# Optimization experiments

Hardware: AMD Instinct MI355X
Metric: run time of the kernel (lower is better)

The kernel has to match this reference:

```python
import jax, jax.numpy as jnp
import numpy as np

N, E = 50000, 800000
HID, HEADS, EDIM = 64, 4, 3
NEG_SLOPE = 0.2
LN_EPS = 1e-5


def setup_inputs() -> dict:
    key = jax.random.key(0)
    ks = jax.random.split(key, 12)
    h = jax.random.normal(ks[0], (N, HID), dtype=jnp.float32)
    edge_index = jax.random.randint(ks[1], (2, E), 0, N, dtype=jnp.int64)
    edge_attr = jax.random.normal(ks[2], (E, EDIM), dtype=jnp.float32)
    t = jax.random.uniform(ks[3], (1,), dtype=jnp.float32)
    s = 1.0 / np.sqrt(HID)
    W = jax.random.normal(ks[4], (HID, HEADS * HID), dtype=jnp.float32) * s
    att_src = jax.random.normal(ks[5], (1, HEADS, HID), dtype=jnp.float32) * s
    att_dst = jax.random.normal(ks[6], (1, HEADS, HID), dtype=jnp.float32) * s
    W_edge = jax.random.normal(ks[7], (EDIM, HEADS * HID), dtype=jnp.float32) * s
    att_edge = jax.random.normal(ks[8], (1, HEADS, HID), dtype=jnp.float32) * s
    bias = jnp.zeros((HID,), dtype=jnp.float32)
    ln_gamma = jnp.ones((HID,), dtype=jnp.float32)
    ln_beta = jnp.zeros((HID,), dtype=jnp.float32)
    return {"t": t, "h": h, "edge_index": edge_index, "edge_attr": edge_attr,
            "W": W, "att_src": att_src, "att_dst": att_dst, "W_edge": W_edge,
            "att_edge": att_edge, "bias": bias, "ln_gamma": ln_gamma, "ln_beta": ln_beta}


def reference(t, h, edge_index, edge_attr, W, att_src, att_dst, W_edge, att_edge, bias, ln_gamma, ln_beta):
    # GATConv (PyG, edge_dim>0, add_self_loops=False, concat=False, eval mode)
    x = (h @ W).reshape(N, HEADS, HID)                     # [N,H,C]
    a_src = (x * att_src).sum(-1)                          # [N,H]
    a_dst = (x * att_dst).sum(-1)                          # [N,H]
    e = (edge_attr @ W_edge).reshape(E, HEADS, HID)        # [E,H,C]
    a_edge = (e * att_edge).sum(-1)                        # [E,H]
    src, dst = edge_index[0], edge_index[1]
    alpha = a_src[src] + a_dst[dst] + a_edge               # [E,H]
    alpha = jax.nn.leaky_relu(alpha, NEG_SLOPE)
    # softmax over edges sharing the same destination node
    amax = jax.ops.segment_max(alpha, dst, num_segments=N)  # [N,H]
    ex = jnp.exp(alpha - amax[dst])
    esum = jax.ops.segment_sum(ex, dst, num_segments=N)     # [N,H]
    alpha = ex / (esum[dst] + 1e-16)
    msg = x[src] * alpha[:, :, None]                        # [E,H,C]
    out = jax.ops.segment_sum(msg, dst, num_segments=N)     # [N,H,C]
    out = out.mean(axis=1) + bias                           # concat=False -> head mean
    # LayerNorm + SiLU
    mu = out.mean(-1, keepdims=True)
    var = ((out - mu) ** 2).mean(-1, keepdims=True)
    y = (out - mu) * jax.lax.rsqrt(var + LN_EPS) * ln_gamma + ln_beta
    return y * jax.nn.sigmoid(y)
```

## Files before the change

kernel.cpp:

```cpp
#include <hip/hip_runtime.h>
#include <hip/hip_bf16.h>

#define HIDC 64
#define NEG_SLOPE 0.2f
#define SCAN_G 128

typedef __hip_bfloat16 bf16;
typedef short bf16x8 __attribute__((ext_vector_type(8)));
typedef float floatx4 __attribute__((ext_vector_type(4)));
typedef int intx4 __attribute__((ext_vector_type(4)));

static __device__ __forceinline__ float b2f(bf16 v) { return __bfloat162float(v); }

static __device__ __forceinline__ unsigned short f2us(float f) {
  bf16 b = __float2bfloat16(f);
  union { bf16 b; unsigned short u; } c;
  c.b = b;
  return c.u;
}

template <bool FF>
static __device__ __forceinline__ float ld(const void* __restrict__ p, size_t i) {
  return FF ? ((const float*)p)[i] : b2f(((const bf16*)p)[i]);
}
static __device__ __forceinline__ float ldr(const void* __restrict__ p, size_t i,
                                            bool ff) {
  return ff ? ((const float*)p)[i] : b2f(((const bf16*)p)[i]);
}
template <bool I64>
static __device__ __forceinline__ int ldi(const int* __restrict__ p, long long i) {
  return I64 ? (int)((const long long*)p)[i] : p[i];
}
static __device__ __forceinline__ int clampN(int v, int N) {
  return ((unsigned)v < (unsigned)N) ? v : 0;
}

static __device__ __forceinline__ int4 ntload4(const int4* __restrict__ p) {
  intx4 v = __builtin_nontemporal_load((const intx4*)p);
  return make_int4(v.x, v.y, v.z, v.w);
}

static __device__ __forceinline__ bool det_f32(const unsigned* __restrict__ hw) {
  unsigned w = hw[threadIdx.x & 31];
  int ex = (w >> 7) & 0xFF;
  unsigned long long b = __ballot(ex >= 99 && ex <= 135);
  return __popcll(b) < 32;
}
static __device__ __forceinline__ bool det_i64(const int* __restrict__ ei) {
  int v = ei[2 * (threadIdx.x & 31) + 1];
  return __ballot(v != 0) == 0ULL;
}

template <bool FF, bool I64>
static __device__ __forceinline__ void xh_body(
    const void* __restrict__ h, const void* __restrict__ W,
    const void* __restrict__ att_src, const void* __restrict__ att_dst,
    const int* __restrict__ ei, bf16* __restrict__ x,
    float* __restrict__ a_src, float* __restrict__ a_dst,
    int* __restrict__ cnt, int* __restrict__ erank, int N, int E,
    unsigned short* __restrict__ hls, unsigned short* __restrict__ wls) {
  for (long long e = (long long)blockIdx.x * 256 + threadIdx.x; e < E;
       e += (long long)gridDim.x * 256) {
    int dst = clampN(ldi<I64>(ei, (long long)E + e), N);
    erank[e] = atomicAdd(&cnt[dst], 1);
  }
  const int t = threadIdx.x;
  const long long n0 = (long long)blockIdx.x * 64;
  {
    const int c = t;
    const int jn = c & 63, hd = c >> 6;
    const int r = hd * 64 + (jn & 3) * 16 + (jn >> 2);
#pragma unroll
    for (int q = 0; q < 8; q++) {
      unsigned short u[8];
#pragma unroll
      for (int j = 0; j < 8; j++) {
        int k = q * 8 + j;
        u[j] = FF ? f2us(((const float*)W)[(size_t)k * 256 + c])
                  : ((const unsigned short*)W)[(size_t)k * 256 + c];
      }
      int4 v = make_int4((int)(u[0] | ((unsigned)u[1] << 16)),
                         (int)(u[2] | ((unsigned)u[3] << 16)),
                         (int)(u[4] | ((unsigned)u[5] << 16)),
                         (int)(u[6] | ((unsigned)u[7] << 16)));
      *(int4*)&wls[r * 64 + (q ^ (r & 7)) * 8] = v;
    }
  }
  {
    const int row = t >> 2;
    const long long n = n0 + row;
#pragma unroll
    for (int dq = 0; dq < 2; dq++) {
      int q = (t & 3) * 2 + dq;
      int4 v;
      if (n < N) {
        if (FF) {
          const float4* hp = (const float4*)h + n * 16 + q * 2;
          float4 f0 = hp[0], f1 = hp[1];
          v = make_int4((int)(f2us(f0.x) | ((unsigned)f2us(f0.y) << 16)),
                        (int)(f2us(f0.z) | ((unsigned)f2us(f0.w) << 16)),
                        (int)(f2us(f1.x) | ((unsigned)f2us(f1.y) << 16)),
                        (int)(f2us(f1.z) | ((unsigned)f2us(f1.w) << 16)));
        } else {
          v = *((const int4*)((const unsigned short*)h + n * 64 + q * 8));
        }
      } else {
        v = make_int4(0, 0, 0, 0);
      }
      *(int4*)&hls[row * 64 + (q ^ (row & 7)) * 8] = v;
    }
  }
  __syncthreads();
  const int w = t >> 6;
  const int lane = t & 63;
  const int lm = lane & 15, lq = lane >> 4;
  bf16x8 af[4][2];
#pragma unroll
  for (int nt = 0; nt < 4; nt++)
#pragma unroll
    for (int ks = 0; ks < 2; ks++) {
      int m = nt * 16 + lm;
      int q = ks * 4 + lq;
      af[nt][ks] = *(const bf16x8*)&hls[m * 64 + (q ^ (m & 7)) * 8];
    }
  floatx4 acc[4][4];
#pragma unroll
  for (int nt = 0; nt < 4; nt++)
#pragma unroll
    for (int ct = 0; ct < 4; ct++) acc[nt][ct] = (floatx4){0.f, 0.f, 0.f, 0.f};
#pragma unroll
  for (int ct = 0; ct < 4; ct++) {
    int c = w * 64 + ct * 16 + lm;
    bf16x8 b0 = *(const bf16x8*)&wls[c * 64 + ((lq) ^ (c & 7)) * 8];
    bf16x8 b1 = *(const bf16x8*)&wls[c * 64 + ((4 + lq) ^ (c & 7)) * 8];
#pragma unroll
    for (int nt = 0; nt < 4; nt++) {
      acc[nt][ct] = __builtin_amdgcn_mfma_f32_16x16x32_bf16(af[nt][0], b0,
                                                            acc[nt][ct], 0, 0, 0);
      acc[nt][ct] = __builtin_amdgcn_mfma_f32_16x16x32_bf16(af[nt][1], b1,
                                                            acc[nt][ct], 0, 0, 0);
    }
  }
  float as_c[4], ad_c[4];
#pragma unroll
  for (int ct = 0; ct < 4; ct++) {
    as_c[ct] = ld<FF>(att_src, w * 64 + lm * 4 + ct);
    ad_c[ct] = ld<FF>(att_dst, w * 64 + lm * 4 + ct);
  }
#pragma unroll
  for (int nt = 0; nt < 4; nt++) {
    float ps[4] = {0.f, 0.f, 0.f, 0.f}, pd[4] = {0.f, 0.f, 0.f, 0.f};
#pragma unroll
    for (int ct = 0; ct < 4; ct++) {
#pragma unroll
      for (int r = 0; r < 4; r++) {
        ps[r] += acc[nt][ct][r] * as_c[ct];
        pd[r] += acc[nt][ct][r] * ad_c[ct];
      }
    }
    long long nb = n0 + nt * 16 + lq * 4;
#pragma unroll
    for (int r = 0; r < 4; r++) {
      long long n = nb + r;
      if (n < N) {
        ushort4 us = make_ushort4(f2us(acc[nt][0][r]), f2us(acc[nt][1][r]),
                                  f2us(acc[nt][2][r]), f2us(acc[nt][3][r]));
        *(ushort4*)&x[n * 256 + w * 64 + lm * 4] = us;
      }
    }
#pragma unroll
    for (int mask = 1; mask < 16; mask <<= 1) {
#pragma unroll
      for (int r = 0; r < 4; r++) {
        ps[r] += __shfl_xor(ps[r], mask);
        pd[r] += __shfl_xor(pd[r], mask);
      }
    }
    if (lm == 0) {
#pragma unroll
      for (int r = 0; r < 4; r++) {
        long long n = nb + r;
        if (n < N) {
          a_src[n * 4 + w] = ps[r];
          a_dst[n * 4 + w] = pd[r];
        }
      }
    }
  }
}

__global__ void __launch_bounds__(256) k_xh(
    const void* __restrict__ h, const void* __restrict__ W,
    const void* __restrict__ att_src, const void* __restrict__ att_dst,
    const int* __restrict__ ei, bf16* __restrict__ x,
    float* __restrict__ a_src, float* __restrict__ a_dst,
    int* __restrict__ cnt, int* __restrict__ erank, int N, int E) {
  __shared__ alignas(16) unsigned short hls[64 * 64];
  __shared__ alignas(16) unsigned short wls[256 * 64];
  bool f32 = det_f32((const unsigned*)h);
  bool i64 = det_i64(ei);
  if (f32) {
    if (i64) xh_body<true, true>(h, W, att_src, att_dst, ei, x, a_src, a_dst, cnt, erank, N, E, hls, wls);
    else     xh_body<true, false>(h, W, att_src, att_dst, ei, x, a_src, a_dst, cnt, erank, N, E, hls, wls);
  } else {
    if (i64) xh_body<false, true>(h, W, att_src, att_dst, ei, x, a_src, a_dst, cnt, erank, N, E, hls, wls);
    else     xh_body<false, false>(h, W, att_src, att_dst, ei, x, a_src, a_dst, cnt, erank, N, E, hls, wls);
  }
}

__global__ void __launch_bounds__(1024) k_bscan(
    const void* __restrict__ W_edge, const void* __restrict__ att_edge,
    const unsigned* __restrict__ hw, const int* __restrict__ cnt,
    int* __restrict__ offs, int* __restrict__ bsum, int* __restrict__ bbase,
    int* __restrict__ done, float* __restrict__ M, int N) {
  int b = blockIdx.x, t = threadIdx.x;
  if (b == 0 && t < 768) {
    bool ff = det_f32(hw);
    int wv = t >> 6, lane = t & 63;
    int d = wv >> 2, hh = wv & 3;
    float p = ldr(W_edge, (size_t)d * 256 + hh * 64 + lane, ff) *
              ldr(att_edge, (size_t)hh * 64 + lane, ff);
#pragma unroll
    for (int o = 32; o; o >>= 1) p += __shfl_down(p, o);
    if (lane == 0) M[d * 4 + hh] = p;
  }
  const int C = (N + SCAN_G - 1) / SCAN_G;
  const int b0 = b * C;
  __shared__ int ts[1024];
  __shared__ int lastf;
  int v = 0;
  if (t < C && b0 + t < N) v = cnt[b0 + t];
  ts[t] = v;
  __syncthreads();
  for (int off = 1; off < 1024; off <<= 1) {
    int u = (t >= off) ? ts[t - off] : 0;
    __syncthreads();
    ts[t] += u;
    __syncthreads();
  }
  if (t < C && b0 + t < N) offs[b0 + t] = ts[t] - v;
  if (t == 1023) {
    atomicExch(&bsum[b], ts[1023]);
    __threadfence();
    int old = atomicAdd(done, 1);
    lastf = (old == SCAN_G - 1) ? 1 : 0;
  }
  __syncthreads();
  if (lastf) {
    int w = (t < SCAN_G) ? atomicAdd(&bsum[t], 0) : 0;
    ts[t] = w;
    __syncthreads();
    for (int off = 1; off < 1024; off <<= 1) {
      int u = (t >= off) ? ts[t - off] : 0;
      __syncthreads();
      ts[t] += u;
      __syncthreads();
    }
    if (t < SCAN_G) bbase[t] = ts[t] - w;
  }
}

template <bool FF, bool I64>
static __device__ __forceinline__ void es_body(
    const int* __restrict__ ei, const void* __restrict__ eattr,
    const float* __restrict__ a_src, const float* __restrict__ a_dst,
    const float* __restrict__ M, const int* __restrict__ offs,
    const int* __restrict__ bbase, const int* __restrict__ erank,
    int4* __restrict__ slots, int E, int N, int C,
    unsigned* __restrict__ sattr) {
  const long long e0 = (long long)blockIdx.x * 256;
  {
    const unsigned bpe = FF ? 12u : 6u;
    const unsigned* gsrc = (const unsigned*)((const char*)eattr + e0 * bpe);
    unsigned ndw = FF ? 768u : 384u;
    long long bytes_left = ((long long)E - e0) * bpe;
    if (bytes_left < 0) bytes_left = 0;
    unsigned max_dw = (unsigned)((bytes_left + 3) >> 2);
    if (ndw > max_dw) ndw = max_dw;
    for (unsigned i = threadIdx.x; i < ndw; i += 256) sattr[i] = gsrc[i];
  }
  __syncthreads();
  long long e = e0 + threadIdx.x;
  if (e >= E) return;
  int src = clampN(ldi<I64>(ei, e), N);
  int dst = clampN(ldi<I64>(ei, (long long)E + e), N);
  int pos = offs[dst] + bbase[dst / C] + erank[e];
  float ea0, ea1, ea2;
  if (FF) {
    const float* sf = (const float*)sattr;
    ea0 = sf[threadIdx.x * 3 + 0];
    ea1 = sf[threadIdx.x * 3 + 1];
    ea2 = sf[threadIdx.x * 3 + 2];
  } else {
    const unsigned short* su = (const unsigned short*)sattr;
    ea0 = __uint_as_float((unsigned)su[threadIdx.x * 3 + 0] << 16);
    ea1 = __uint_as_float((unsigned)su[threadIdx.x * 3 + 1] << 16);
    ea2 = __uint_as_float((unsigned)su[threadIdx.x * 3 + 2] << 16);
  }
  const float4 m0 = ((const float4*)M)[0];
  const float4 m1 = ((const float4*)M)[1];
  const float4 m2 = ((const float4*)M)[2];
  const float4 as4 = ((const float4*)a_src)[src];
  const float4 ad4 = ((const float4*)a_dst)[dst];
  float al[4];
  al[0] = as4.x + ad4.x + ea0 * m0.x + ea1 * m1.x + ea2 * m2.x;
  al[1] = as4.y + ad4.y + ea0 * m0.y + ea1 * m1.y + ea2 * m2.y;
  al[2] = as4.z + ad4.z + ea0 * m0.z + ea1 * m1.z + ea2 * m2.z;
  al[3] = as4.w + ad4.w + ea0 * m0.w + ea1 * m1.w + ea2 * m2.w;
  unsigned short u[4];
#pragma unroll
  for (int hh = 0; hh < 4; hh++) {
    float a = al[hh];
    a = (a > 0.f) ? a : NEG_SLOPE * a;
    a = fminf(fmaxf(a, -60.f), 60.f);
    u[hh] = f2us(__expf(a));
  }
  slots[pos] = make_int4(src, (int)(u[0] | ((unsigned)u[1] << 16)),
                         (int)(u[2] | ((unsigned)u[3] << 16)), 0);
}

__global__ void __launch_bounds__(256) k_es(
    const int* __restrict__ ei, const void* __restrict__ eattr,
    const float* __restrict__ a_src, const float* __restrict__ a_dst,
    const float* __restrict__ M, const unsigned* __restrict__ hw,
    const int* __restrict__ offs, const int* __restrict__ bbase,
    const int* __restrict__ erank, int4* __restrict__ slots, int E, int N,
    int C) {
  __shared__ unsigned sattr[768];
  bool f32 = det_f32(hw);
  bool i64 = det_i64(ei);
  if (f32) {
    if (i64) es_body<true, true>(ei, eattr, a_src, a_dst, M, offs, bbase, erank, slots, E, N, C, sattr);
    else     es_body<true, false>(ei, eattr, a_src, a_dst, M, offs, bbase, erank, slots, E, N, C, sattr);
  } else {
    if (i64) es_body<false, true>(ei, eattr, a_src, a_dst, M, offs, bbase, erank, slots, E, N, C, sattr);
    else     es_body<false, false>(ei, eattr, a_src, a_dst, M, offs, bbase, erank, slots, E, N, C, sattr);
  }
}

static __device__ __forceinline__ uint2 xgat(const uint2* __restrict__ xr,
                                             int src, int lane) {
  int ss = __builtin_amdgcn_readfirstlane(src);
  return xr[(size_t)(unsigned)ss * 64 + lane];
}

__global__ void __launch_bounds__(256) k_agg(
    const int* __restrict__ offs, const int* __restrict__ bbase,
    const int4* __restrict__ slots, const unsigned* __restrict__ xu,
    const unsigned* __restrict__ hw, const void* __restrict__ bias,
    const void* __restrict__ gamma, const void* __restrict__ beta,
    void* __restrict__ out, int N, int E, int C) {
  const int t = threadIdx.x;
  const int wv = t >> 6, lane = t & 63;
  const int n = blockIdx.x * 4 + wv;
  if (n >= N) return;
  const int head2 = lane >> 5;
  const unsigned wshift = (lane & 16) ? 0u : 16u;
  const uint2* __restrict__ xr = (const uint2*)xu;

  int s0 = __builtin_amdgcn_readfirstlane(offs[n] + bbase[n / C]);
  int s1 = (n + 1 < N)
               ? __builtin_amdgcn_readfirstlane(offs[n + 1] + bbase[(n + 1) / C])
               : E;

  float a0 = 0.f, a1 = 0.f, a2 = 0.f, a3 = 0.f, ws = 0.f;

#define ACC4(q, d)                                                    \
  do {                                                                \
    unsigned ee = head2 ? (unsigned)(q).z : (unsigned)(q).y;          \
    float wv_ = __uint_as_float((ee << wshift) & 0xffff0000u);        \
    a0 += wv_ * __uint_as_float((d).x << 16);                         \
    a1 += wv_ * __uint_as_float((d).x & 0xffff0000u);                 \
    a2 += wv_ * __uint_as_float((d).y << 16);                         \
    a3 += wv_ * __uint_as_float((d).y & 0xffff0000u);                 \
    ws += wv_;                                                        \
  } while (0)

  int i = s0;
  for (; i + 8 <= s1; i += 8) {
    int4 q0 = ntload4(&slots[i + 0]);
    int4 q1 = ntload4(&slots[i + 1]);
    int4 q2 = ntload4(&slots[i + 2]);
    int4 q3 = ntload4(&slots[i + 3]);
    int4 q4 = ntload4(&slots[i + 4]);
    int4 q5 = ntload4(&slots[i + 5]);
    int4 q6 = ntload4(&slots[i + 6]);
    int4 q7 = ntload4(&slots[i + 7]);
    uint2 d0 = xgat(xr, q0.x, lane);
    uint2 d1 = xgat(xr, q1.x, lane);
    uint2 d2 = xgat(xr, q2.x, lane);
    uint2 d3 = xgat(xr, q3.x, lane);
    uint2 d4 = xgat(xr, q4.x, lane);
    uint2 d5 = xgat(xr, q5.x, lane);
    uint2 d6 = xgat(xr, q6.x, lane);
    uint2 d7 = xgat(xr, q7.x, lane);
    ACC4(q0, d0); ACC4(q1, d1); ACC4(q2, d2); ACC4(q3, d3);
    ACC4(q4, d4); ACC4(q5, d5); ACC4(q6, d6); ACC4(q7, d7);
  }
  for (; i + 4 <= s1; i += 4) {
    int4 q0 = ntload4(&slots[i + 0]);
    int4 q1 = ntload4(&slots[i + 1]);
    int4 q2 = ntload4(&slots[i + 2]);
    int4 q3 = ntload4(&slots[i + 3]);
    uint2 d0 = xgat(xr, q0.x, lane);
    uint2 d1 = xgat(xr, q1.x, lane);
    uint2 d2 = xgat(xr, q2.x, lane);
    uint2 d3 = xgat(xr, q3.x, lane);
    ACC4(q0, d0); ACC4(q1, d1); ACC4(q2, d2); ACC4(q3, d3);
  }
  for (; i < s1; i++) {
    int4 q = ntload4(&slots[i]);
    uint2 d = xgat(xr, q.x, lane);
    ACC4(q, d);
  }
#undef ACC4

  float inv = 1.f / (ws + 1e-16f);
  float v0 = a0 * inv, v1 = a1 * inv, v2 = a2 * inv, v3 = a3 * inv;
  v0 += __shfl_xor(v0, 16); v1 += __shfl_xor(v1, 16);
  v2 += __shfl_xor(v2, 16); v3 += __shfl_xor(v3, 16);
  v0 += __shfl_xor(v0, 32); v1 += __shfl_xor(v1, 32);
  v2 += __shfl_xor(v2, 32); v3 += __shfl_xor(v3, 32);

  bool ff = det_f32(hw);
  const int c0 = (lane & 15) * 4;
  float m0 = v0 * 0.25f + ldr(bias, c0 + 0, ff);
  float m1 = v1 * 0.25f + ldr(bias, c0 + 1, ff);
  float m2 = v2 * 0.25f + ldr(bias, c0 + 2, ff);
  float m3 = v3 * 0.25f + ldr(bias, c0 + 3, ff);

  float s = (m0 + m1) + (m2 + m3);
  s += __shfl_xor(s, 1); s += __shfl_xor(s, 2);
  s += __shfl_xor(s, 4); s += __shfl_xor(s, 8);
  float mu = s * 0.015625f;
  float d0 = m0 - mu, d1 = m1 - mu, d2 = m2 - mu, d3 = m3 - mu;
  float vq = (d0 * d0 + d1 * d1) + (d2 * d2 + d3 * d3);
  vq += __shfl_xor(vq, 1); vq += __shfl_xor(vq, 2);
  vq += __shfl_xor(vq, 4); vq += __shfl_xor(vq, 8);
  float rstd = rsqrtf(vq * 0.015625f + 1e-5f);

  if ((lane >> 4) == 0) {
    float y0 = d0 * rstd * ldr(gamma, c0 + 0, ff) + ldr(beta, c0 + 0, ff);
    float y1 = d1 * rstd * ldr(gamma, c0 + 1, ff) + ldr(beta, c0 + 1, ff);
    float y2 = d2 * rstd * ldr(gamma, c0 + 2, ff) + ldr(beta, c0 + 2, ff);
    float y3 = d3 * rstd * ldr(gamma, c0 + 3, ff) + ldr(beta, c0 + 3, ff);
    float r0 = y0 / (1.f + __expf(-y0));
    float r1 = y1 / (1.f + __expf(-y1));
    float r2 = y2 / (1.f + __expf(-y2));
    float r3 = y3 / (1.f + __expf(-y3));
    size_t ob = (size_t)n * 64 + c0;
    if (ff) {
      *(float4*)((float*)out + ob) = make_float4(r0, r1, r2, r3);
    } else {
      *(ushort4*)((bf16*)out + ob) =
          make_ushort4(f2us(r0), f2us(r1), f2us(r2), f2us(r3));
    }
  }
}

extern "C" void kernel_launch(void* const* d_in, const int* in_sizes, int n_in,
                              void* d_out, int out_size, void* d_ws,
                              size_t ws_size, hipStream_t stream) {
  const void* h        = d_in[1];
  const int*  ei       = (const int*)d_in[2];
  const void* eattr    = d_in[3];
  const void* W        = d_in[4];
  const void* att_src  = d_in[5];
  const void* att_dst  = d_in[6];
  const void* W_edge   = d_in[7];
  const void* att_edge = d_in[8];
  const void* bias     = d_in[9];
  const void* gamma    = d_in[10];
  const void* beta     = d_in[11];

  const int N = in_sizes[1] / HIDC;
  const int E = in_sizes[3] / 3;
  const int C = (N + SCAN_G - 1) / SCAN_G;

  char* p = (char*)d_ws;
  float* M    = (float*)p; p += 64;
  bf16* x     = (bf16*)p;  p += (size_t)N * 256 * 2;
  float* asrc = (float*)p; p += (size_t)N * 4 * 4;
  float* adst = (float*)p; p += (size_t)N * 4 * 4;
  int4* slots = (int4*)p;  p += (size_t)E * 16;
  int* cnt    = (int*)p;   p += (size_t)N * 4;
  int* done   = (int*)p;   p += 64;
  int* offs   = (int*)p;   p += ((size_t)N + 4) * 4;
  int* erank  = (int*)p;   p += (size_t)E * 4;
  int* bsum   = (int*)p;   p += SCAN_G * 4;
  int* bbase  = (int*)p;   p += SCAN_G * 4;

  size_t need = (size_t)(p - (char*)d_ws);
  if (ws_size < need || N <= 0 || E <= 0) {
    hipMemsetAsync(d_out, 0, (size_t)out_size * 2, stream);
    return;
  }

  hipMemsetAsync(cnt, 0, (size_t)N * 4 + 64, stream);

  k_xh<<<(N + 63) / 64, 256, 0, stream>>>(h, W, att_src, att_dst, ei, x,
                                          asrc, adst, cnt, erank, N, E);
  k_bscan<<<SCAN_G, 1024, 0, stream>>>(W_edge, att_edge, (const unsigned*)h,
                                       cnt, offs, bsum, bbase, done, M, N);
  k_es<<<(E + 255) / 256, 256, 0, stream>>>(ei, eattr, asrc, adst, M,
                                            (const unsigned*)h, offs, bbase,
                                            erank, slots, E, N, C);
  k_agg<<<(N + 3) / 4, 256, 0, stream>>>(offs, bbase, slots, (const unsigned*)x,
                                         (const unsigned*)h, bias, gamma, beta,
                                         d_out, N, E, C);
}
```

Measured before the change: 243.4 us.

## Fuse degree scan and edge-attention projection into the node transform kernel

Removes the separate block-scan kernel. The last block to finish the node-transform kernel, detected with an atomic done counter, now runs the per-destination offset scan serially per thread. Block 0 of the same kernel computes the edge-attention projection M. Destination counters are padded to 64 bytes each to cut atomic contention on shared cache lines, and SCAN_G is raised to 256. This saves a kernel launch and the memory round trip between kernels, but it leaves a long serial scan in a single block at the tail, and the padding makes the memset 16x larger.

```diff
diff --git a/kernel.cpp b/kernel.cpp
--- a/kernel.cpp
+++ b/kernel.cpp
@@ -3,7 +3,7 @@
 
 #define HIDC 64
 #define NEG_SLOPE 0.2f
-#define SCAN_G 128
+#define SCAN_G 256
 
 typedef __hip_bfloat16 bf16;
 typedef short bf16x8 __attribute__((ext_vector_type(8)));
@@ -55,16 +55,76 @@
 static __device__ __forceinline__ void xh_body(
     const void* __restrict__ h, const void* __restrict__ W,
     const void* __restrict__ att_src, const void* __restrict__ att_dst,
+    const void* __restrict__ W_edge, const void* __restrict__ att_edge,
     const int* __restrict__ ei, bf16* __restrict__ x,
     float* __restrict__ a_src, float* __restrict__ a_dst,
-    int* __restrict__ cnt, int* __restrict__ erank, int N, int E,
+    float* __restrict__ M, int* __restrict__ cnt, int* __restrict__ erank,
+    int* __restrict__ offs, int* __restrict__ bbase, int* __restrict__ done,
+    int N, int E, int C,
     unsigned short* __restrict__ hls, unsigned short* __restrict__ wls) {
-  for (long long e = (long long)blockIdx.x * 256 + threadIdx.x; e < E;
+  const int t = threadIdx.x;
+  if (blockIdx.x == 0) {
+    int wv = t >> 6, lane = t & 63;
+#pragma unroll
+    for (int d = 0; d < 3; d++) {
+      float pM = ld<FF>(W_edge, (size_t)d * 256 + wv * 64 + lane) *
+                 ld<FF>(att_edge, (size_t)wv * 64 + lane);
+#pragma unroll
+      for (int o = 32; o; o >>= 1) pM += __shfl_down(pM, o);
+      if (lane == 0) M[d * 4 + wv] = pM;
+    }
+  }
+  for (long long e = (long long)blockIdx.x * 256 + t; e < E;
        e += (long long)gridDim.x * 256) {
     int dst = clampN(ldi<I64>(ei, (long long)E + e), N);
-    erank[e] = atomicAdd(&cnt[dst], 1);
-  }
-  const int t = threadIdx.x;
+    erank[e] = atomicAdd(&cnt[(size_t)dst * 16], 1);
+  }
+  __syncthreads();
+  if (t == 0) {
+    __threadfence();
+    int old = atomicAdd(done, 1);
+    ((int*)hls)[0] = (old == (int)gridDim.x - 1) ? 1 : 0;
+  }
+  __syncthreads();
+  bool last = ((int*)hls)[0] != 0;
+  __syncthreads();
+  if (last) {
+    int* sb = (int*)wls;
+    const int base = t * C;
+    int run = 0;
+    int j = 0;
+    for (; j + 8 <= C; j += 8) {
+      int v[8];
+#pragma unroll
+      for (int k = 0; k < 8; k++) {
+        int idx = base + j + k;
+        v[k] = (idx < N) ? atomicAdd(&cnt[(size_t)idx * 16], 0) : 0;
+      }
+#pragma unroll
+      for (int k = 0; k < 8; k++) {
+        int idx = base + j + k;
+        if (idx < N) offs[idx] = run;
+        run += v[k];
+      }
+    }
+    for (; j < C; j++) {
+      int idx = base + j;
+      int v = (idx < N) ? atomicAdd(&cnt[(size_t)idx * 16], 0) : 0;
+      if (idx < N) offs[idx] = run;
+      run += v;
+    }
+    sb[t] = run;
+    int tot = run;
+    __syncthreads();
+    for (int off = 1; off < 256; off <<= 1) {
+      int u = (t >= off) ? sb[t - off] : 0;
+      __syncthreads();
+      sb[t] += u;
+      __syncthreads();
+    }
+    bbase[t] = sb[t] - tot;
+    __syncthreads();
+  }
   const long long n0 = (long long)blockIdx.x * 64;
   {
     const int c = t;
@@ -192,71 +252,22 @@
 __global__ void __launch_bounds__(256) k_xh(
     const void* __restrict__ h, const void* __restrict__ W,
     const void* __restrict__ att_src, const void* __restrict__ att_dst,
+    const void* __restrict__ W_edge, const void* __restrict__ att_edge,
     const int* __restrict__ ei, bf16* __restrict__ x,
     float* __restrict__ a_src, float* __restrict__ a_dst,
-    int* __restrict__ cnt, int* __restrict__ erank, int N, int E) {
+    float* __restrict__ M, int* __restrict__ cnt, int* __restrict__ erank,
+    int* __restrict__ offs, int* __restrict__ bbase, int* __restrict__ done,
+    int N, int E, int C) {
   __shared__ alignas(16) unsigned short hls[64 * 64];
   __shared__ alignas(16) unsigned short wls[256 * 64];
   bool f32 = det_f32((const unsigned*)h);
   bool i64 = det_i64(ei);
   if (f32) {
-    if (i64) xh_body<true, true>(h, W, att_src, att_dst, ei, x, a_src, a_dst, cnt, erank, N, E, hls, wls);
-    else     xh_body<true, false>(h, W, att_src, att_dst, ei, x, a_src, a_dst, cnt, erank, N, E, hls, wls);
+    if (i64) xh_body<true, true>(h, W, att_src, att_dst, W_edge, att_edge, ei, x, a_src, a_dst, M, cnt, erank, offs, bbase, done, N, E, C, hls, wls);
+    else     xh_body<true, false>(h, W, att_src, att_dst, W_edge, att_edge, ei, x, a_src, a_dst, M, cnt, erank, offs, bbase, done, N, E, C, hls, wls);
   } else {
-    if (i64) xh_body<false, true>(h, W, att_src, att_dst, ei, x, a_src, a_dst, cnt, erank, N, E, hls, wls);
-    else     xh_body<false, false>(h, W, att_src, att_dst, ei, x, a_src, a_dst, cnt, erank, N, E, hls, wls);
-  }
-}
-
-__global__ void __launch_bounds__(1024) k_bscan(
-    const void* __restrict__ W_edge, const void* __restrict__ att_edge,
-    const unsigned* __restrict__ hw, const int* __restrict__ cnt,
-    int* __restrict__ offs, int* __restrict__ bsum, int* __restrict__ bbase,
-    int* __restrict__ done, float* __restrict__ M, int N) {
-  int b = blockIdx.x, t = threadIdx.x;
-  if (b == 0 && t < 768) {
-    bool ff = det_f32(hw);
-    int wv = t >> 6, lane = t & 63;
-    int d = wv >> 2, hh = wv & 3;
-    float p = ldr(W_edge, (size_t)d * 256 + hh * 64 + lane, ff) *
-              ldr(att_edge, (size_t)hh * 64 + lane, ff);
-#pragma unroll
-    for (int o = 32; o; o >>= 1) p += __shfl_down(p, o);
-    if (lane == 0) M[d * 4 + hh] = p;
-  }
-  const int C = (N + SCAN_G - 1) / SCAN_G;
-  const int b0 = b * C;
-  __shared__ int ts[1024];
-  __shared__ int lastf;
-  int v = 0;
-  if (t < C && b0 + t < N) v = cnt[b0 + t];
-  ts[t] = v;
-  __syncthreads();
-  for (int off = 1; off < 1024; off <<= 1) {
-    int u = (t >= off) ? ts[t - off] : 0;
-    __syncthreads();
-    ts[t] += u;
-    __syncthreads();
-  }
-  if (t < C && b0 + t < N) offs[b0 + t] = ts[t] - v;
-  if (t == 1023) {
-    atomicExch(&bsum[b], ts[1023]);
-    __threadfence();
-    int old = atomicAdd(done, 1);
-    lastf = (old == SCAN_G - 1) ? 1 : 0;
-  }
-  __syncthreads();
-  if (lastf) {
-    int w = (t < SCAN_G) ? atomicAdd(&bsum[t], 0) : 0;
-    ts[t] = w;
-    __syncthreads();
-    for (int off = 1; off < 1024; off <<= 1) {
-      int u = (t >= off) ? ts[t - off] : 0;
-      __syncthreads();
-      ts[t] += u;
-      __syncthreads();
-    }
-    if (t < SCAN_G) bbase[t] = ts[t] - w;
+    if (i64) xh_body<false, true>(h, W, att_src, att_dst, W_edge, att_edge, ei, x, a_src, a_dst, M, cnt, erank, offs, bbase, done, N, E, C, hls, wls);
+    else     xh_body<false, false>(h, W, att_src, att_dst, W_edge, att_edge, ei, x, a_src, a_dst, M, cnt, erank, offs, bbase, done, N, E, C, hls, wls);
   }
 }
 
@@ -483,11 +494,10 @@
   float* asrc = (float*)p; p += (size_t)N * 4 * 4;
   float* adst = (float*)p; p += (size_t)N * 4 * 4;
   int4* slots = (int4*)p;  p += (size_t)E * 16;
-  int* cnt    = (int*)p;   p += (size_t)N * 4;
+  int* cnt    = (int*)p;   p += (size_t)N * 64;
   int* done   = (int*)p;   p += 64;
   int* offs   = (int*)p;   p += ((size_t)N + 4) * 4;
   int* erank  = (int*)p;   p += (size_t)E * 4;
-  int* bsum   = (int*)p;   p += SCAN_G * 4;
   int* bbase  = (int*)p;   p += SCAN_G * 4;
 
   size_t need = (size_t)(p - (char*)d_ws);
@@ -496,12 +506,11 @@
     return;
   }
 
-  hipMemsetAsync(cnt, 0, (size_t)N * 4 + 64, stream);
-
-  k_xh<<<(N + 63) / 64, 256, 0, stream>>>(h, W, att_src, att_dst, ei, x,
-                                          asrc, adst, cnt, erank, N, E);
-  k_bscan<<<SCAN_G, 1024, 0, stream>>>(W_edge, att_edge, (const unsigned*)h,
-                                       cnt, offs, bsum, bbase, done, M, N);
+  hipMemsetAsync(cnt, 0, (size_t)N * 64 + 64, stream);
+
+  k_xh<<<(N + 63) / 64, 256, 0, stream>>>(h, W, att_src, att_dst, W_edge,
+                                          att_edge, ei, x, asrc, adst, M, cnt,
+                                          erank, offs, bbase, done, N, E, C);
   k_es<<<(E + 255) / 256, 256, 0, stream>>>(ei, eattr, asrc, adst, M,
                                             (const unsigned*)h, offs, bbase,
                                             erank, slots, E, N, C);
```

New measurement: 353.6 us. 1.45x slower.
